# Kernel tuning notes

Hardware: AMD Instinct MI355X
Metric: run time of the kernel (lower is better)

Reference implementation:

```python
import jax, jax.numpy as jnp
import numpy as np

N, E, B = 400000, 800000, 16384
MAX_DEG = 10  # PyG MFConv default max_degree -> 11 weight sets
EPS = 1e-5


def setup_inputs() -> dict:
    key = jax.random.key(0)
    ks = jax.random.split(key, 32)
    d = {}
    d["x"] = jax.random.normal(ks[0], (N, 8), jnp.float32)
    d["edge_index"] = jax.random.randint(ks[1], (2, E), 0, N)
    d["batch"] = jnp.sort(jax.random.randint(ks[2], (N,), 0, B))
    d["x_mord"] = jax.random.normal(ks[3], (B, 862), jnp.float32)
    D = MAX_DEG + 1
    # MFConv degree-dependent weights: Wl (with bias) applied to neighbor sum, Wr (no bias) to self.
    d["Wl1"] = jax.random.normal(ks[4], (D, 32, 8), jnp.float32) * 0.2
    d["bl1"] = jnp.zeros((D, 32), jnp.float32)
    d["Wr1"] = jax.random.normal(ks[5], (D, 32, 8), jnp.float32) * 0.2
    d["Wl2"] = jax.random.normal(ks[6], (D, 32, 32), jnp.float32) * 0.1
    d["bl2"] = jnp.zeros((D, 32), jnp.float32)
    d["Wr2"] = jax.random.normal(ks[7], (D, 32, 32), jnp.float32) * 0.1
    d["Wl3"] = jax.random.normal(ks[8], (D, 32, 32), jnp.float32) * 0.1
    d["bl3"] = jnp.zeros((D, 32), jnp.float32)
    d["Wr3"] = jax.random.normal(ks[9], (D, 32, 32), jnp.float32) * 0.1
    # Dense MLP head
    d["W_fc1"] = jax.random.normal(ks[10], (512, 862), jnp.float32) * 0.03
    d["b_fc1"] = jnp.zeros((512,), jnp.float32)
    d["g1"] = jnp.ones((512,), jnp.float32)
    d["be1"] = jnp.zeros((512,), jnp.float32)
    d["W_fc2"] = jax.random.normal(ks[11], (128, 512), jnp.float32) * 0.04
    d["b_fc2"] = jnp.zeros((128,), jnp.float32)
    d["g2"] = jnp.ones((128,), jnp.float32)
    d["be2"] = jnp.zeros((128,), jnp.float32)
    d["W_fc3"] = jax.random.normal(ks[12], (64, 128), jnp.float32) * 0.09
    d["b_fc3"] = jnp.zeros((64,), jnp.float32)
    d["g3"] = jnp.ones((64,), jnp.float32)
    d["be3"] = jnp.zeros((64,), jnp.float32)
    d["W_out"] = jax.random.normal(ks[13], (1, 96), jnp.float32) * 0.1
    d["b_out"] = jnp.zeros((1,), jnp.float32)
    return d


def _mfconv(x, src, dst, deg_idx, Wl, bl, Wr):
    # h_i = sum_{j in N(i)} x_j  (source_to_target aggregation)
    h = jax.ops.segment_sum(x[src], dst, num_segments=x.shape[0])
    Wl_n = Wl[deg_idx]   # [N, out, in]
    Wr_n = Wr[deg_idx]
    return (jnp.einsum('noi,ni->no', Wl_n, h) + bl[deg_idx]
            + jnp.einsum('noi,ni->no', Wr_n, x))


def _bn_train(h, g, b):
    mu = jnp.mean(h, axis=0)
    var = jnp.mean((h - mu) ** 2, axis=0)  # biased, as torch BN training
    return (h - mu) * jax.lax.rsqrt(var + EPS) * g + b


def reference(x, edge_index, batch, x_mord,
              Wl1, bl1, Wr1, Wl2, bl2, Wr2, Wl3, bl3, Wr3,
              W_fc1, b_fc1, g1, be1, W_fc2, b_fc2, g2, be2,
              W_fc3, b_fc3, g3, be3, W_out, b_out):
    src, dst = edge_index[0], edge_index[1]
    n = x.shape[0]
    deg = jax.ops.segment_sum(jnp.ones((src.shape[0],), jnp.float32), dst, num_segments=n)
    deg_idx = jnp.minimum(deg, MAX_DEG).astype(jnp.int32)

    h = jax.nn.relu(_mfconv(x, src, dst, deg_idx, Wl1, bl1, Wr1))
    h = jax.nn.relu(_mfconv(h, src, dst, deg_idx, Wl2, bl2, Wr2))
    h = _mfconv(h, src, dst, deg_idx, Wl3, bl3, Wr3)

    # global mean pool over graphs
    num_graphs = x_mord.shape[0]
    sums = jax.ops.segment_sum(h, batch, num_segments=num_graphs)
    cnts = jax.ops.segment_sum(jnp.ones((n,), jnp.float32), batch, num_segments=num_graphs)
    pooled = sums / jnp.maximum(cnts, 1.0)[:, None]  # [B, 32]

    m = _bn_train(jax.nn.relu(x_mord @ W_fc1.T + b_fc1), g1, be1)
    m = _bn_train(jax.nn.relu(m @ W_fc2.T + b_fc2), g2, be2)
    m = _bn_train(jax.nn.relu(m @ W_fc3.T + b_fc3), g3, be3)

    z = jnp.concatenate([pooled, m], axis=1)  # [B, 96]
    return jax.nn.sigmoid(z @ W_out.T + b_out)
```

## Files before the change

kernel.cpp:

```cpp
#include <hip/hip_runtime.h>
#include <hip/hip_bf16.h>
#include <math.h>

#define MORD 862

typedef short s16x8 __attribute__((ext_vector_type(8)));
typedef float f32x4 __attribute__((ext_vector_type(4)));
typedef float f32x4a __attribute__((ext_vector_type(4), aligned(4)));

static __device__ __forceinline__ unsigned short f2bf(float v) {
  __hip_bfloat16 h = __float2bfloat16(v);
  return *(unsigned short*)&h;
}
static __device__ __forceinline__ float bf2f(unsigned short u) {
  unsigned int x = ((unsigned int)u) << 16;
  return *(float*)&x;
}

__global__ __launch_bounds__(512) void bin_scan(const int* __restrict__ bhist, int* __restrict__ boff,
                                                int* __restrict__ gcur, int nbins, int E) {
  __shared__ int ts[512];
  int tid = threadIdx.x;
  int v = (tid < nbins) ? bhist[tid] : 0;
  ts[tid] = v;
  __syncthreads();
  for (int st = 1; st < 512; st <<= 1) {
    int t = (tid >= st) ? ts[tid - st] : 0;
    __syncthreads();
    ts[tid] += t;
    __syncthreads();
  }
  int ex = ts[tid] - v;
  if (tid < nbins) { boff[tid] = ex; gcur[tid] = ex; }
  if (tid == 0) boff[nbins] = E;
}

__global__ __launch_bounds__(256) void bin_split(const int* __restrict__ srcA, const int* __restrict__ dstA,
                                                 int* __restrict__ gcur, unsigned long long* __restrict__ ebuf,
                                                 int E, int nbins) {
  __shared__ unsigned long long sbuf[512 * 8];
  __shared__ int lcur[512];
  int tid = threadIdx.x;
  for (int base = blockIdx.x * 1024; base < E; base += (int)gridDim.x * 1024) {
    for (int i = tid; i < nbins; i += 256) lcur[i] = 0;
    __syncthreads();
    int e0 = base + tid * 4;
#pragma unroll
    for (int j = 0; j < 4; j++) {
      int e = e0 + j;
      if (e < E) {
        int d = dstA[e], s = srcA[e];
        int bin = d >> 10;
        unsigned long long p = ((unsigned long long)(unsigned int)d << 32) | (unsigned int)s;
        int slot = atomicAdd(&lcur[bin], 1);
        if (slot < 8) sbuf[bin * 8 + slot] = p;
        else { int g = atomicAdd(&gcur[bin], 1); ebuf[g] = p; }
      }
    }
    __syncthreads();
    for (int b = tid; b < nbins; b += 256) {
      int cnt = min(lcur[b], 8);
      if (cnt > 0) {
        int g = atomicAdd(&gcur[b], cnt);
        for (int k = 0; k < cnt; k++) ebuf[g + k] = sbuf[b * 8 + k];
      }
    }
    __syncthreads();
  }
}

__global__ __launch_bounds__(256) void bin_csr(const unsigned long long* __restrict__ ebuf,
                                               const int* __restrict__ boff,
                                               int* __restrict__ off, int* __restrict__ csr,
                                               int N, int E) {
  __shared__ int lcur[1024];
  __shared__ int part[256];
  int b = blockIdx.x;
  int n0 = b << 10;
  int nn = min(1024, N - n0);
  int e0 = boff[b], e1 = boff[b + 1];
  int tid = threadIdx.x;
  for (int i = tid; i < nn; i += 256) lcur[i] = 0;
  __syncthreads();
  for (int e = e0 + tid; e < e1; e += 256) {
    int d = (int)(ebuf[e] >> 32);
    atomicAdd(&lcur[d - n0], 1);
  }
  __syncthreads();
  int base4 = tid * 4;
  int c0 = (base4 < nn) ? lcur[base4] : 0;
  int c1 = (base4 + 1 < nn) ? lcur[base4 + 1] : 0;
  int c2 = (base4 + 2 < nn) ? lcur[base4 + 2] : 0;
  int c3 = (base4 + 3 < nn) ? lcur[base4 + 3] : 0;
  int tot = c0 + c1 + c2 + c3;
  part[tid] = tot;
  __syncthreads();
  for (int st = 1; st < 256; st <<= 1) {
    int t = (tid >= st) ? part[tid - st] : 0;
    __syncthreads();
    part[tid] += t;
    __syncthreads();
  }
  int pre = part[tid] - tot;
  __syncthreads();
  if (base4 < nn)     { lcur[base4]     = pre;                off[n0 + base4]     = e0 + pre; }
  if (base4 + 1 < nn) { lcur[base4 + 1] = pre + c0;           off[n0 + base4 + 1] = e0 + pre + c0; }
  if (base4 + 2 < nn) { lcur[base4 + 2] = pre + c0 + c1;      off[n0 + base4 + 2] = e0 + pre + c0 + c1; }
  if (base4 + 3 < nn) { lcur[base4 + 3] = pre + c0 + c1 + c2; off[n0 + base4 + 3] = e0 + pre + c0 + c1 + c2; }
  if (b == 0 && tid == 0) off[N] = E;
  __syncthreads();
  for (int e = e0 + tid; e < e1; e += 256) {
    unsigned long long p = ebuf[e];
    int d = (int)(p >> 32);
    int s = (int)(p & 0xffffffffu);
    int slot = atomicAdd(&lcur[d - n0], 1);
    csr[e0 + slot] = s;
  }
}

__global__ __launch_bounds__(256) void mega_prep(const int* __restrict__ dstA, int* __restrict__ bhist, int E, int nbins,
                                                 const float* __restrict__ Wl1, const float* __restrict__ Wr1,
                                                 unsigned short* __restrict__ Wc1,
                                                 const float* __restrict__ Wl2, const float* __restrict__ Wr2,
                                                 unsigned short* __restrict__ Wc2,
                                                 const float* __restrict__ Wl3, const float* __restrict__ Wr3,
                                                 unsigned short* __restrict__ Wc3,
                                                 const int* __restrict__ batch, int* __restrict__ goff, int N, int B,
                                                 const float* __restrict__ Wf1, unsigned short* __restrict__ Bbf1) {
  if (blockIdx.y == 0) {
    if (blockIdx.x >= 400) return;
    __shared__ int lh[512];
    for (int i = threadIdx.x; i < nbins; i += 256) lh[i] = 0;
    __syncthreads();
    for (int e = blockIdx.x * 256 + threadIdx.x; e < E; e += 400 * 256)
      atomicAdd(&lh[dstA[e] >> 10], 1);
    __syncthreads();
    for (int i = threadIdx.x; i < nbins; i += 256)
      if (lh[i]) atomicAdd(&bhist[i], lh[i]);
    return;
  }
  int bx = blockIdx.x;
  if (bx >= 330) {
    int idx = (bx - 330) * 256 + threadIdx.x;
    if (idx >= 512 * 224) return;
    int r = idx / 224, c4 = (idx % 224) * 4;
#pragma unroll
    for (int j = 0; j < 4; j++) {
      int k = c4 + j;
      float v = (k < MORD) ? Wf1[(size_t)r * MORD + k] : 0.f;
      Bbf1[(size_t)r * 896 + k] = f2bf(v);
    }
    return;
  }
  if (bx >= 264) {
    int b = (bx - 264) * 256 + threadIdx.x;
    if (b > B) return;
    int lo = 0, hi = N;
    while (lo < hi) {
      int mid = (lo + hi) >> 1;
      if (batch[mid] < b) lo = mid + 1; else hi = mid;
    }
    goff[b] = lo;
    return;
  }
  int set = bx / 88;
  const float* Wl = set == 0 ? Wl1 : (set == 1 ? Wl2 : Wl3);
  const float* Wr = set == 0 ? Wr1 : (set == 1 ? Wr2 : Wr3);
  unsigned short* Wc = set == 0 ? Wc1 : (set == 1 ? Wc2 : Wc3);
  int CIN = set == 0 ? 8 : 32;
  int idx = (bx - set * 88) * 256 + threadIdx.x;
  if (idx >= 352 * 64) return;
  int row = idx >> 6, k = idx & 63;
  int d = row >> 5, o = row & 31;
  float v = 0.f;
  if (k < CIN) v = Wl[((size_t)d * 32 + o) * CIN + k];
  else if (k < 2 * CIN) v = Wr[((size_t)d * 32 + o) * CIN + (k - CIN)];
  Wc[idx] = f2bf(v);
}

__global__ __launch_bounds__(256) void prep_hx1(const float* __restrict__ x, const int* __restrict__ off,
                                                const int* __restrict__ csr,
                                                unsigned short* __restrict__ x1, unsigned short* __restrict__ agg1, int N) {
  int n = blockIdx.x * 256 + threadIdx.x;
  if (n >= N) return;
  int a = off[n], b = off[n + 1];
  float ag[8] = {};
  for (int base = a; base < b; base += 4) {
    int rem = b - base;
    int j1 = base + (rem > 1 ? 1 : 0);
    int j2 = base + (rem > 2 ? 2 : 0);
    int j3 = base + (rem > 3 ? 3 : 0);
    int cc0 = csr[base], cc1 = csr[j1], cc2 = csr[j2], cc3 = csr[j3];
    f32x4a v0a = *(const f32x4a*)(x + (size_t)cc0 * 8);
    f32x4a v0b = *(const f32x4a*)(x + (size_t)cc0 * 8 + 4);
    f32x4a v1a = *(const f32x4a*)(x + (size_t)cc1 * 8);
    f32x4a v1b = *(const f32x4a*)(x + (size_t)cc1 * 8 + 4);
    f32x4a v2a = *(const f32x4a*)(x + (size_t)cc2 * 8);
    f32x4a v2b = *(const f32x4a*)(x + (size_t)cc2 * 8 + 4);
    f32x4a v3a = *(const f32x4a*)(x + (size_t)cc3 * 8);
    f32x4a v3b = *(const f32x4a*)(x + (size_t)cc3 * 8 + 4);
    float m1 = rem > 1 ? 1.f : 0.f;
    float m2 = rem > 2 ? 1.f : 0.f;
    float m3 = rem > 3 ? 1.f : 0.f;
#pragma unroll
    for (int t = 0; t < 4; t++) {
      ag[t] += v0a[t];
      ag[t] = fmaf(m1, v1a[t], ag[t]);
      ag[t] = fmaf(m2, v2a[t], ag[t]);
      ag[t] = fmaf(m3, v3a[t], ag[t]);
      ag[t + 4] += v0b[t];
      ag[t + 4] = fmaf(m1, v1b[t], ag[t + 4]);
      ag[t + 4] = fmaf(m2, v2b[t], ag[t + 4]);
      ag[t + 4] = fmaf(m3, v3b[t], ag[t + 4]);
    }
  }
  const float* xo = x + (size_t)n * 8;
  s16x8 w0, w1;
#pragma unroll
  for (int t = 0; t < 8; t++) {
    w0[t] = (short)f2bf(ag[t]);
    w1[t] = (short)f2bf(xo[t]);
  }
  *(s16x8*)(agg1 + (size_t)n * 8) = w0;
  *(s16x8*)(x1 + (size_t)n * 8) = w1;
}

__global__ __launch_bounds__(256) void gather_c(const unsigned short* __restrict__ X, const int* __restrict__ off,
                                                const int* __restrict__ csr, unsigned short* __restrict__ AGG, int N) {
  long long tid = (long long)blockIdx.x * 256 + threadIdx.x;
  if (tid >= (long long)N * 4) return;
  int n = (int)(tid >> 2), q = (int)(tid & 3);
  int a = off[n], b = off[n + 1];
  float s[8] = {};
  for (int base = a; base < b; base += 4) {
    int rem = b - base;
    int j1 = base + (rem > 1 ? 1 : 0);
    int j2 = base + (rem > 2 ? 2 : 0);
    int j3 = base + (rem > 3 ? 3 : 0);
    int cc0 = csr[base], cc1 = csr[j1], cc2 = csr[j2], cc3 = csr[j3];
    const s16x8 v0 = *(const s16x8*)(X + (size_t)cc0 * 32 + q * 8);
    const s16x8 v1 = *(const s16x8*)(X + (size_t)cc1 * 32 + q * 8);
    const s16x8 v2 = *(const s16x8*)(X + (size_t)cc2 * 32 + q * 8);
    const s16x8 v3 = *(const s16x8*)(X + (size_t)cc3 * 32 + q * 8);
    float m1 = rem > 1 ? 1.f : 0.f;
    float m2 = rem > 2 ? 1.f : 0.f;
    float m3 = rem > 3 ? 1.f : 0.f;
#pragma unroll
    for (int t = 0; t < 8; t++) {
      s[t] += bf2f((unsigned short)v0[t]);
      s[t] = fmaf(m1, bf2f((unsigned short)v1[t]), s[t]);
      s[t] = fmaf(m2, bf2f((unsigned short)v2[t]), s[t]);
      s[t] = fmaf(m3, bf2f((unsigned short)v3[t]), s[t]);
    }
  }
  s16x8 w;
#pragma unroll
  for (int t = 0; t < 8; t++) w[t] = (short)f2bf(s[t]);
  *(s16x8*)(AGG + (size_t)n * 32 + q * 8) = w;
}

template <int KS, int ACH, int OUTMODE>
__global__ __launch_bounds__(512, 4) void mfconv_mfma(const unsigned short* __restrict__ xin,
                                                      const unsigned short* __restrict__ agg,
                                                      const unsigned short* __restrict__ Wcat,
                                                      const float* __restrict__ bl,
                                                      const int* __restrict__ off,
                                                      unsigned short* __restrict__ outp, int N) {
  __shared__ __align__(16) unsigned short As[128 * ACH * 8];
  __shared__ __align__(16) unsigned short Bs[352 * 64];
  __shared__ float sbias[352];
  __shared__ int sdeg[128];
  const int tid = threadIdx.x;
  const int wid = tid >> 6, lane = tid & 63;

  for (int s = wid; s < 44; s += 8) {
    int c = s * 64 + lane;
    int cs = c ^ ((c >> 3) & 7);
    __builtin_amdgcn_global_load_lds((const __attribute__((address_space(1))) void*)((const char*)Wcat + (size_t)cs * 16),
                                     (__attribute__((address_space(3))) void*)((char*)Bs + s * 1024), 16, 0, 0);
  }
  for (int i = tid; i < 352; i += 512) sbias[i] = bl[i];

  const int ntiles = N >> 7;
  for (int t = blockIdx.x; t < ntiles; t += (int)gridDim.x) {
    const int row0 = t << 7;
    __syncthreads();
    for (int s = wid; s < 2 * ACH; s += 8) {
      int c = s * 64 + lane;
      int row = c / ACH, ch = c & (ACH - 1);
      int cs = ch ^ (row & (ACH - 1));
      size_t grow = (size_t)(row0 + row);
      const char* srcp;
      if (ACH == 4) {
        srcp = (cs == 1) ? (const char*)xin + grow * 16 : (const char*)agg + grow * 16;
      } else {
        srcp = (cs < 4) ? (const char*)agg + grow * 64 + (size_t)cs * 16
                        : (const char*)xin + grow * 64 + (size_t)(cs - 4) * 16;
      }
      __builtin_amdgcn_global_load_lds((const __attribute__((address_space(1))) void*)srcp,
                                       (__attribute__((address_space(3))) void*)((char*)As + s * 1024), 16, 0, 0);
    }
    if (tid < 128) sdeg[tid] = min(off[row0 + tid + 1] - off[row0 + tid], 10);
    __syncthreads();

    const int ra = wid * 16 + (lane & 15);
    const int g4 = lane >> 4;
    const int rl0 = wid * 16 + g4 * 4;
    int dj[4];
#pragma unroll
    for (int j = 0; j < 4; j++) dj[j] = sdeg[rl0 + j];

#pragma unroll
    for (int h = 0; h < 2; h++) {
      f32x4 acc[11] = {};
#pragma unroll
      for (int kk = 0; kk < KS; kk++) {
        int cha = (kk * 4 + g4) ^ (ra & (ACH - 1));
        s16x8 af = *(const s16x8*)((const char*)As + (size_t)(ra * ACH + cha) * 16);
#pragma unroll
        for (int nn = 0; nn < 11; nn++) {
          int rb = (h * 11 + nn) * 16 + (lane & 15);
          int cb = rb * 8 + kk * 4 + g4;
          s16x8 bf = *(const s16x8*)((const char*)Bs + (size_t)(cb ^ (rb & 7)) * 16);
          acc[nn] = __builtin_amdgcn_mfma_f32_16x16x32_bf16(af, bf, acc[nn], 0, 0, 0);
        }
      }
#pragma unroll
      for (int nn = 0; nn < 11; nn++) {
        int n = h * 11 + nn;
        int dsel = n >> 1;
        int o = (n & 1) * 16 + (lane & 15);
        float bv = sbias[dsel * 32 + o];
#pragma unroll
        for (int j = 0; j < 4; j++) {
          if (dj[j] == dsel) {
            float v = acc[nn][j] + bv;
            size_t gr = (size_t)row0 + rl0 + j;
            if (OUTMODE == 0) v = fmaxf(v, 0.f);
            outp[gr * 32 + o] = f2bf(v);
          }
        }
      }
    }
  }
}

__global__ __launch_bounds__(256) void cvtA(const float* __restrict__ xm, unsigned short* __restrict__ Abf, int B) {
  const int q = 224;
  int t = blockIdx.x * 256 + threadIdx.x;
  if (t >= B * q) return;
  int r = t / q, c4 = (t % q) * 4;
#pragma unroll
  for (int j = 0; j < 4; j++) {
    int k = c4 + j;
    float v = (k < MORD) ? xm[(size_t)r * MORD + k] : 0.f;
    Abf[(size_t)r * 896 + k] = f2bf(v);
  }
}

__global__ __launch_bounds__(256) void gemm_fc1b(const unsigned short* __restrict__ A,
                                                 const unsigned short* __restrict__ Bw,
                                                 const float* __restrict__ bias,
                                                 unsigned short* __restrict__ Cout,
                                                 float* __restrict__ csum, float* __restrict__ csq,
                                                 int M, int Nn, int Kp) {
  __shared__ __align__(16) unsigned short As[128 * 64];
  __shared__ __align__(16) unsigned short Bs[128 * 64];
  __shared__ float scs[128], sqs[128];
  int tid = threadIdx.x;
  int wid = tid >> 6, lane = tid & 63;
  int lin = blockIdx.x + blockIdx.y * 4;
  int swz = (lin & 7) * 64 + (lin >> 3);
  int m0 = (swz >> 2) * 128, n0 = (swz & 3) * 128;
  int wr = wid >> 1, wc = wid & 1;
  f32x4 acc[4][4] = {};

  int srow_l = lane >> 3;
  int scol = (lane & 7) * 8;
  int aReadBase = ((wr * 64 + (lane & 15)) * 128) + ((lane >> 4) * 16);
  int bReadBase = ((wc * 64 + (lane & 15)) * 128) + ((lane >> 4) * 16);

  const unsigned short* Ablk = A + (size_t)m0 * Kp;
  const unsigned short* Bblk = Bw + (size_t)n0 * Kp;

  for (int k0 = 0; k0 < Kp; k0 += 64) {
#pragma unroll
    for (int i = 0; i < 4; i++) {
      int s = wid * 4 + i;
      int row = s * 8 + srow_l;
      const unsigned short* ga = Ablk + (size_t)row * Kp + k0 + scol;
      const unsigned short* gb = Bblk + (size_t)row * Kp + k0 + scol;
      __builtin_amdgcn_global_load_lds((const __attribute__((address_space(1))) void*)ga,
                                       (__attribute__((address_space(3))) void*)(As + s * 512), 16, 0, 0);
      __builtin_amdgcn_global_load_lds((const __attribute__((address_space(1))) void*)gb,
                                       (__attribute__((address_space(3))) void*)(Bs + s * 512), 16, 0, 0);
    }
    __syncthreads();
#pragma unroll
    for (int kk = 0; kk < 2; kk++) {
      s16x8 af[4], bfr[4];
#pragma unroll
      for (int m = 0; m < 4; m++)
        af[m] = *(const s16x8*)((const char*)As + aReadBase + m * (16 * 128) + kk * 64);
#pragma unroll
      for (int n = 0; n < 4; n++)
        bfr[n] = *(const s16x8*)((const char*)Bs + bReadBase + n * (16 * 128) + kk * 64);
#pragma unroll
      for (int m = 0; m < 4; m++)
#pragma unroll
        for (int n = 0; n < 4; n++)
          acc[m][n] = __builtin_amdgcn_mfma_f32_16x16x32_bf16(af[m], bfr[n], acc[m][n], 0, 0, 0);
    }
    __syncthreads();
  }

  if (tid < 128) { scs[tid] = 0.f; sqs[tid] = 0.f; }
  __syncthreads();
  int rbase = m0 + wr * 64 + (lane >> 4) * 4;
  int lc = lane & 15;
#pragma unroll
  for (int n = 0; n < 4; n++) {
    int colb = wc * 64 + n * 16 + lc;
    float bv = bias[n0 + colb];
    float s = 0.f, q = 0.f;
#pragma unroll
    for (int m = 0; m < 4; m++) {
#pragma unroll
      for (int j = 0; j < 4; j++) {
        int row = rbase + m * 16 + j;
        float v = fmaxf(acc[m][n][j] + bv, 0.f);
        Cout[(size_t)row * Nn + n0 + colb] = f2bf(v);
        s += v;
        q = fmaf(v, v, q);
      }
    }
    s += __shfl_xor(s, 16); q += __shfl_xor(q, 16);
    s += __shfl_xor(s, 32); q += __shfl_xor(q, 32);
    if ((lane >> 4) == 0) { atomicAdd(&scs[colb], s); atomicAdd(&sqs[colb], q); }
  }
  __syncthreads();
  if (tid < 128) { atomicAdd(&csum[n0 + tid], scs[tid]); atomicAdd(&csq[n0 + tid], sqs[tid]); }
}

__global__ __launch_bounds__(256) void prepW2_bn(const float* __restrict__ W2, const float* __restrict__ b2,
                                                 const float* __restrict__ s1, const float* __restrict__ q1,
                                                 const float* __restrict__ g1, const float* __restrict__ be1,
                                                 unsigned short* __restrict__ W2p, float* __restrict__ b2p,
                                                 int Nn, int K, float invM) {
  __shared__ float a1l[512], h1l[512];
  for (int c = threadIdx.x; c < K; c += 256) {
    float mu = s1[c] * invM;
    float var = q1[c] * invM - mu * mu;
    float sc = g1[c] * rsqrtf(var + 1e-5f);
    a1l[c] = sc;
    h1l[c] = be1[c] - mu * sc;
  }
  __syncthreads();
  int wid = threadIdx.x >> 6, lane = threadIdx.x & 63;
  int n = blockIdx.x * 4 + wid;
  if (n >= Nn) return;
  float part = 0.f;
  for (int k = lane; k < K; k += 64) {
    float w = W2[(size_t)n * K + k];
    W2p[(size_t)n * K + k] = f2bf(w * a1l[k]);
    part = fmaf(w, h1l[k], part);
  }
#pragma unroll
  for (int off = 32; off > 0; off >>= 1) part += __shfl_down(part, off, 64);
  if (lane == 0) b2p[n] = b2[n] + part;
}

__global__ __launch_bounds__(256) void gemm_fc2(const unsigned short* __restrict__ A,
                                                const unsigned short* __restrict__ Bw,
                                                const float* __restrict__ bias,
                                                float* __restrict__ Cout,
                                                float* __restrict__ csum, float* __restrict__ csq,
                                                int M, int Nn, int Kp) {
  __shared__ __align__(16) unsigned short As[128 * 64];
  __shared__ __align__(16) unsigned short Bs[128 * 64];
  __shared__ float scs[128], sqs[128];
  int tid = threadIdx.x;
  int wid = tid >> 6, lane = tid & 63;
  int m0 = blockIdx.y * 128;
  int wr = wid >> 1, wc = wid & 1;
  f32x4 acc[4][4] = {};

  int srow_l = lane >> 3;
  int scol = (lane & 7) * 8;
  int aReadBase = ((wr * 64 + (lane & 15)) * 128) + ((lane >> 4) * 16);
  int bReadBase = ((wc * 64 + (lane & 15)) * 128) + ((lane >> 4) * 16);

  const unsigned short* Ablk = A + (size_t)m0 * Kp;

  for (int k0 = 0; k0 < Kp; k0 += 64) {
#pragma unroll
    for (int i = 0; i < 4; i++) {
      int s = wid * 4 + i;
      int row = s * 8 + srow_l;
      const unsigned short* ga = Ablk + (size_t)row * Kp + k0 + scol;
      const unsigned short* gb = Bw + (size_t)row * Kp + k0 + scol;
      __builtin_amdgcn_global_load_lds((const __attribute__((address_space(1))) void*)ga,
                                       (__attribute__((address_space(3))) void*)(As + s * 512), 16, 0, 0);
      __builtin_amdgcn_global_load_lds((const __attribute__((address_space(1))) void*)gb,
                                       (__attribute__((address_space(3))) void*)(Bs + s * 512), 16, 0, 0);
    }
    __syncthreads();
#pragma unroll
    for (int kk = 0; kk < 2; kk++) {
      s16x8 af[4], bfr[4];
#pragma unroll
      for (int m = 0; m < 4; m++)
        af[m] = *(const s16x8*)((const char*)As + aReadBase + m * (16 * 128) + kk * 64);
#pragma unroll
      for (int n = 0; n < 4; n++)
        bfr[n] = *(const s16x8*)((const char*)Bs + bReadBase + n * (16 * 128) + kk * 64);
#pragma unroll
      for (int m = 0; m < 4; m++)
#pragma unroll
        for (int n = 0; n < 4; n++)
          acc[m][n] = __builtin_amdgcn_mfma_f32_16x16x32_bf16(af[m], bfr[n], acc[m][n], 0, 0, 0);
    }
    __syncthreads();
  }

  if (tid < 128) { scs[tid] = 0.f; sqs[tid] = 0.f; }
  __syncthreads();
  int rbase = m0 + wr * 64 + (lane >> 4) * 4;
  int lc = lane & 15;
#pragma unroll
  for (int n = 0; n < 4; n++) {
    int colb = wc * 64 + n * 16 + lc;
    float bv = bias[colb];
    float s = 0.f, q = 0.f;
#pragma unroll
    for (int m = 0; m < 4; m++) {
#pragma unroll
      for (int j = 0; j < 4; j++) {
        int row = rbase + m * 16 + j;
        float v = fmaxf(acc[m][n][j] + bv, 0.f);
        Cout[(size_t)row * Nn + colb] = v;
        s += v;
        q = fmaf(v, v, q);
      }
    }
    s += __shfl_xor(s, 16); q += __shfl_xor(q, 16);
    s += __shfl_xor(s, 32); q += __shfl_xor(q, 32);
    if ((lane >> 4) == 0) { atomicAdd(&scs[colb], s); atomicAdd(&sqs[colb], q); }
  }
  __syncthreads();
  if (tid < 128) { atomicAdd(&csum[tid], scs[tid]); atomicAdd(&csq[tid], sqs[tid]); }
}

__global__ __launch_bounds__(256) void gemm_fc3(const float* __restrict__ A, const float* __restrict__ Bw,
                                                const float* __restrict__ bias,
                                                const float* __restrict__ s2v, const float* __restrict__ q2v,
                                                const float* __restrict__ g2, const float* __restrict__ be2,
                                                float* __restrict__ C, float* __restrict__ s3, float* __restrict__ q3,
                                                int M, float invM) {
  const int BM = 64, BN = 64, BK = 16, K = 128;
  __shared__ float As[BK][BM + 1];
  __shared__ float Bs[BK][BN + 1];
  __shared__ float a2l[128], h2l[128];
  __shared__ float scs[64], sqs[64];
  int tid = threadIdx.x;
  for (int c = tid; c < 128; c += 256) {
    float mu = s2v[c] * invM;
    float var = q2v[c] * invM - mu * mu;
    float sc = g2[c] * rsqrtf(var + 1e-5f);
    a2l[c] = sc;
    h2l[c] = be2[c] - mu * sc;
  }
  if (tid < 64) { scs[tid] = 0.f; sqs[tid] = 0.f; }
  __syncthreads();
  int bm = blockIdx.y * BM;
  int tr = tid / 16, tc = tid % 16;
  float acc[4][4] = {};
  for (int k0 = 0; k0 < K; k0 += BK) {
    for (int i = tid; i < BM * BK; i += 256) {
      int m = i / BK, k = i % BK;
      float v = A[(size_t)(bm + m) * K + k0 + k];
      As[k][m] = fmaf(v, a2l[k0 + k], h2l[k0 + k]);
    }
    for (int i = tid; i < BN * BK; i += 256) {
      int n = i / BK, k = i % BK;
      Bs[k][n] = Bw[(size_t)n * K + k0 + k];
    }
    __syncthreads();
#pragma unroll
    for (int k = 0; k < BK; k++) {
      float a4[4], b4[4];
#pragma unroll
      for (int xx = 0; xx < 4; xx++) a4[xx] = As[k][tr * 4 + xx];
#pragma unroll
      for (int yy = 0; yy < 4; yy++) b4[yy] = Bs[k][tc * 4 + yy];
#pragma unroll
      for (int xx = 0; xx < 4; xx++)
#pragma unroll
        for (int yy = 0; yy < 4; yy++) acc[xx][yy] = fmaf(a4[xx], b4[yy], acc[xx][yy]);
    }
    __syncthreads();
  }
#pragma unroll
  for (int yy = 0; yy < 4; yy++) {
    int n = tc * 4 + yy;
    float bv = bias[n];
    float s = 0.f, q = 0.f;
#pragma unroll
    for (int xx = 0; xx < 4; xx++) {
      int m = bm + tr * 4 + xx;
      float v = fmaxf(acc[xx][yy] + bv, 0.f);
      C[(size_t)m * 64 + n] = v;
      s += v;
      q = fmaf(v, v, q);
    }
    atomicAdd(&scs[n], s);
    atomicAdd(&sqs[n], q);
  }
  __syncthreads();
  if (tid < 64) { atomicAdd(&s3[tid], scs[tid]); atomicAdd(&q3[tid], sqs[tid]); }
}

__global__ __launch_bounds__(256) void pool_head(const unsigned short* __restrict__ H3, const int* __restrict__ goff,
                                                 const float* __restrict__ m3,
                                                 const float* __restrict__ s3, const float* __restrict__ q3,
                                                 const float* __restrict__ g3, const float* __restrict__ be3,
                                                 const float* __restrict__ Wout, const float* __restrict__ bout,
                                                 float* __restrict__ out, int B, float invM) {
  __shared__ float a3l[64], h3l[64];
  if (threadIdx.x < 64) {
    int c = threadIdx.x;
    float mu = s3[c] * invM;
    float var = q3[c] * invM - mu * mu;
    float sc = g3[c] * rsqrtf(var + 1e-5f);
    a3l[c] = sc;
    h3l[c] = be3[c] - mu * sc;
  }
  __syncthreads();
  int w = (int)((blockIdx.x * 256 + threadIdx.x) >> 6);
  if (w >= B) return;
  int lane = threadIdx.x & 63;
  int c = lane & 31, r2 = lane >> 5;
  int a = goff[w], b = goff[w + 1];
  float s = 0.f;
  for (int r = a + r2; r < b; r += 2) s += bf2f(H3[(size_t)r * 32 + c]);
  s += __shfl_down(s, 32);
  float val = 0.f;
  if (r2 == 0) val = (s / fmaxf((float)(b - a), 1.f)) * Wout[c];
  float mv = m3[(size_t)w * 64 + lane];
  val += fmaf(mv, a3l[lane], h3l[lane]) * Wout[32 + lane];
#pragma unroll
  for (int off = 32; off > 0; off >>= 1) val += __shfl_down(val, off);
  if (lane == 0) out[w] = 1.f / (1.f + expf(-(val + bout[0])));
}

extern "C" void kernel_launch(void* const* d_in, const int* in_sizes, int n_in,
                              void* d_out, int out_size, void* d_ws, size_t ws_size,
                              hipStream_t stream) {
  const float* x = (const float*)d_in[0];
  const int* eidx = (const int*)d_in[1];
  const int* batch = (const int*)d_in[2];
  const float* xmord = (const float*)d_in[3];
  const float* Wl1 = (const float*)d_in[4];
  const float* bl1 = (const float*)d_in[5];
  const float* Wr1 = (const float*)d_in[6];
  const float* Wl2 = (const float*)d_in[7];
  const float* bl2 = (const float*)d_in[8];
  const float* Wr2 = (const float*)d_in[9];
  const float* Wl3 = (const float*)d_in[10];
  const float* bl3 = (const float*)d_in[11];
  const float* Wr3 = (const float*)d_in[12];
  const float* Wf1 = (const float*)d_in[13];
  const float* bf1 = (const float*)d_in[14];
  const float* g1 = (const float*)d_in[15];
  const float* be1 = (const float*)d_in[16];
  const float* Wf2 = (const float*)d_in[17];
  const float* bf2 = (const float*)d_in[18];
  const float* g2 = (const float*)d_in[19];
  const float* be2 = (const float*)d_in[20];
  const float* Wf3 = (const float*)d_in[21];
  const float* bf3 = (const float*)d_in[22];
  const float* g3 = (const float*)d_in[23];
  const float* be3 = (const float*)d_in[24];
  const float* Wout = (const float*)d_in[25];
  const float* bout = (const float*)d_in[26];
  float* out = (float*)d_out;

  const int N = in_sizes[2];
  const int E = in_sizes[1] / 2;
  const int B = in_sizes[3] / MORD;
  const int nbins = (N + 1023) >> 10;
  const int* src = eidx;
  const int* dst = eidx + E;

  char* ws = (char*)d_ws;
  size_t off_ = 0;
  auto alloc = [&](size_t bytes) { size_t o = off_; off_ += (bytes + 255) & ~(size_t)255; return o; };
  size_t oX1 = alloc((size_t)N * 8 * 2);
  size_t oAGG1 = alloc((size_t)N * 8 * 2);
  size_t oX2 = alloc((size_t)N * 32 * 2);
  size_t oX3 = alloc((size_t)N * 32 * 2);
  size_t oAGG = alloc((size_t)N * 32 * 2);
  size_t oOff = alloc((size_t)(N + 1) * 4);
  size_t oCsr = alloc((size_t)E * 4);
  size_t oEbuf = alloc((size_t)E * 8);
  size_t oH3 = alloc((size_t)N * 32 * 2);
  size_t oGoff = alloc((size_t)(B + 1) * 4);
  size_t oStats = alloc(8192 * 4);
  size_t oWc1 = alloc(352 * 64 * 2);
  size_t oWc2 = alloc(352 * 64 * 2);
  size_t oWc3 = alloc(352 * 64 * 2);
  size_t oBbf1 = alloc(512 * 896 * 2);
  size_t oW2p = alloc(128 * 512 * 2 + 1024);
  (void)ws_size;

  unsigned short* X1 = (unsigned short*)(ws + oX1);
  unsigned short* AGG1 = (unsigned short*)(ws + oAGG1);
  unsigned short* X2 = (unsigned short*)(ws + oX2);
  unsigned short* X3 = (unsigned short*)(ws + oX3);
  unsigned short* AGG = (unsigned short*)(ws + oAGG);
  int* offp = (int*)(ws + oOff);
  int* csr = (int*)(ws + oCsr);
  unsigned long long* ebuf = (unsigned long long*)(ws + oEbuf);
  unsigned short* H3 = (unsigned short*)(ws + oH3);
  int* goff = (int*)(ws + oGoff);
  float* st = (float*)(ws + oStats);
  int* bhist = (int*)(st + 4096);
  int* boff = (int*)(st + 4608);
  int* gcur = (int*)(st + 5184);
  unsigned short* Wc1 = (unsigned short*)(ws + oWc1);
  unsigned short* Wc2 = (unsigned short*)(ws + oWc2);
  unsigned short* Wc3 = (unsigned short*)(ws + oWc3);
  unsigned short* Bbf1 = (unsigned short*)(ws + oBbf1);
  unsigned short* W2p = (unsigned short*)(ws + oW2p);
  float* b2p = (float*)(ws + oW2p + 131072);
  float *s1 = st, *q1 = st + 512;
  float *s2 = st + 2048, *q2 = st + 2176;
  float *s3 = st + 2560, *q3 = st + 2624;

  unsigned short* Abf = (unsigned short*)(ws + oX2);
  unsigned short* m1 = (unsigned short*)(ws + oAGG);
  float* m2 = (float*)(ws + oAGG + 16777216);
  float* m3 = (float*)(ws + oOff);

  hipMemsetAsync(st, 0, 4608 * 4, stream);

  mega_prep<<<dim3(778, 2), 256, 0, stream>>>(dst, bhist, E, nbins,
                                              Wl1, Wr1, Wc1, Wl2, Wr2, Wc2, Wl3, Wr3, Wc3,
                                              batch, goff, N, B, Wf1, Bbf1);
  bin_scan<<<1, 512, 0, stream>>>(bhist, boff, gcur, nbins, E);
  bin_split<<<400, 256, 0, stream>>>(src, dst, gcur, ebuf, E, nbins);
  bin_csr<<<nbins, 256, 0, stream>>>(ebuf, boff, offp, csr, N, E);

  prep_hx1<<<(N + 255) / 256, 256, 0, stream>>>(x, offp, csr, X1, AGG1, N);
  mfconv_mfma<1, 4, 0><<<512, 512, 0, stream>>>(X1, AGG1, Wc1, bl1, offp, X2, N);
  gather_c<<<(int)(((long long)N * 4 + 255) / 256), 256, 0, stream>>>(X2, offp, csr, AGG, N);
  mfconv_mfma<2, 8, 0><<<512, 512, 0, stream>>>(X2, AGG, Wc2, bl2, offp, X3, N);
  gather_c<<<(int)(((long long)N * 4 + 255) / 256), 256, 0, stream>>>(X3, offp, csr, AGG, N);
  mfconv_mfma<2, 8, 1><<<512, 512, 0, stream>>>(X3, AGG, Wc3, bl3, offp, H3, N);

  cvtA<<<(B * 224 + 255) / 256, 256, 0, stream>>>(xmord, Abf, B);
  gemm_fc1b<<<dim3(4, B / 128), 256, 0, stream>>>(Abf, Bbf1, bf1, m1, s1, q1, B, 512, 896);
  prepW2_bn<<<32, 256, 0, stream>>>(Wf2, bf2, s1, q1, g1, be1, W2p, b2p, 128, 512, 1.f / B);
  gemm_fc2<<<dim3(1, B / 128), 256, 0, stream>>>(m1, W2p, b2p, m2, s2, q2, B, 128, 512);
  gemm_fc3<<<dim3(1, B / 64), 256, 0, stream>>>(m2, Wf3, bf3, s2, q2, g2, be2, m3, s3, q3, B, 1.f / B);
  pool_head<<<(B * 64 + 255) / 256, 256, 0, stream>>>(H3, goff, m3, s3, q3, g3, be3, Wout, bout, out, B, 1.f / B);
}
```

Before: 327.0 us.

## Sort nodes by degree so MFConv tiles compute only needed weight sets

Adds a degree histogram in bin_csr, a tiny scan, and a permutation kernel that groups nodes by clamped degree. The MFConv MFMA kernels then load rows through this permutation and loop only over the degree range present in each 128-row tile, instead of computing all 11 weight sets and masking. This cuts MFMA work about elevenfold, at the cost of two extra launches, indirect gathers for A rows, and scattered output stores.

```diff
diff --git a/kernel.cpp b/kernel.cpp
--- a/kernel.cpp
+++ b/kernel.cpp
@@ -72,15 +72,18 @@
 __global__ __launch_bounds__(256) void bin_csr(const unsigned long long* __restrict__ ebuf,
                                                const int* __restrict__ boff,
                                                int* __restrict__ off, int* __restrict__ csr,
+                                               int* __restrict__ dcnt,
                                                int N, int E) {
   __shared__ int lcur[1024];
   __shared__ int part[256];
+  __shared__ int ldc[11];
   int b = blockIdx.x;
   int n0 = b << 10;
   int nn = min(1024, N - n0);
   int e0 = boff[b], e1 = boff[b + 1];
   int tid = threadIdx.x;
   for (int i = tid; i < nn; i += 256) lcur[i] = 0;
+  if (tid < 11) ldc[tid] = 0;
   __syncthreads();
   for (int e = e0 + tid; e < e1; e += 256) {
     int d = (int)(ebuf[e] >> 32);
@@ -93,6 +96,10 @@
   int c2 = (base4 + 2 < nn) ? lcur[base4 + 2] : 0;
   int c3 = (base4 + 3 < nn) ? lcur[base4 + 3] : 0;
   int tot = c0 + c1 + c2 + c3;
+  if (base4 < nn) atomicAdd(&ldc[min(c0, 10)], 1);
+  if (base4 + 1 < nn) atomicAdd(&ldc[min(c1, 10)], 1);
+  if (base4 + 2 < nn) atomicAdd(&ldc[min(c2, 10)], 1);
+  if (base4 + 3 < nn) atomicAdd(&ldc[min(c3, 10)], 1);
   part[tid] = tot;
   __syncthreads();
   for (int st = 1; st < 256; st <<= 1) {
@@ -109,12 +116,52 @@
   if (base4 + 3 < nn) { lcur[base4 + 3] = pre + c0 + c1 + c2; off[n0 + base4 + 3] = e0 + pre + c0 + c1 + c2; }
   if (b == 0 && tid == 0) off[N] = E;
   __syncthreads();
+  if (tid < 11 && ldc[tid]) atomicAdd(&dcnt[tid], ldc[tid]);
   for (int e = e0 + tid; e < e1; e += 256) {
     unsigned long long p = ebuf[e];
     int d = (int)(p >> 32);
     int s = (int)(p & 0xffffffffu);
     int slot = atomicAdd(&lcur[d - n0], 1);
     csr[e0 + slot] = s;
+  }
+}
+
+__global__ void scan11(const int* __restrict__ dcnt, int* __restrict__ dcur) {
+  if (threadIdx.x == 0) {
+    int run = 0;
+    for (int d = 0; d < 11; d++) { dcur[d] = run; run += dcnt[d]; }
+  }
+}
+
+__global__ __launch_bounds__(256) void perm_scatter(const int* __restrict__ off, int* __restrict__ dcur,
+                                                    int* __restrict__ perm, int* __restrict__ degp, int N) {
+  __shared__ int ldc[11];
+  __shared__ int lbase[11];
+  int tid = threadIdx.x;
+  if (tid < 11) ldc[tid] = 0;
+  __syncthreads();
+  int n0 = blockIdx.x * 1024;
+  int d[4], slot[4];
+#pragma unroll
+  for (int j = 0; j < 4; j++) {
+    int n = n0 + tid * 4 + j;
+    d[j] = -1;
+    if (n < N) {
+      d[j] = min(off[n + 1] - off[n], 10);
+      slot[j] = atomicAdd(&ldc[d[j]], 1);
+    }
+  }
+  __syncthreads();
+  if (tid < 11) lbase[tid] = ldc[tid] ? atomicAdd(&dcur[tid], ldc[tid]) : 0;
+  __syncthreads();
+#pragma unroll
+  for (int j = 0; j < 4; j++) {
+    int n = n0 + tid * 4 + j;
+    if (n < N) {
+      int p = lbase[d[j]] + slot[j];
+      perm[p] = n;
+      degp[p] = d[j];
+    }
   }
 }
 
@@ -264,12 +311,12 @@
                                                       const unsigned short* __restrict__ agg,
                                                       const unsigned short* __restrict__ Wcat,
                                                       const float* __restrict__ bl,
-                                                      const int* __restrict__ off,
+                                                      const int* __restrict__ perm,
+                                                      const int* __restrict__ degp,
                                                       unsigned short* __restrict__ outp, int N) {
   __shared__ __align__(16) unsigned short As[128 * ACH * 8];
   __shared__ __align__(16) unsigned short Bs[352 * 64];
   __shared__ float sbias[352];
-  __shared__ int sdeg[128];
   const int tid = threadIdx.x;
   const int wid = tid >> 6, lane = tid & 63;
 
@@ -281,6 +328,11 @@
   }
   for (int i = tid; i < 352; i += 512) sbias[i] = bl[i];
 
+  const int ra = wid * 16 + (lane & 15);
+  const int g4 = lane >> 4;
+  const int lc = lane & 15;
+  const int rl0 = wid * 16 + g4 * 4;
+
   const int ntiles = N >> 7;
   for (int t = blockIdx.x; t < ntiles; t += (int)gridDim.x) {
     const int row0 = t << 7;
@@ -289,56 +341,52 @@
       int c = s * 64 + lane;
       int row = c / ACH, ch = c & (ACH - 1);
       int cs = ch ^ (row & (ACH - 1));
-      size_t grow = (size_t)(row0 + row);
+      size_t g = (size_t)perm[row0 + row];
       const char* srcp;
       if (ACH == 4) {
-        srcp = (cs == 1) ? (const char*)xin + grow * 16 : (const char*)agg + grow * 16;
+        srcp = (cs == 1) ? (const char*)xin + g * 16 : (const char*)agg + g * 16;
       } else {
-        srcp = (cs < 4) ? (const char*)agg + grow * 64 + (size_t)cs * 16
-                        : (const char*)xin + grow * 64 + (size_t)(cs - 4) * 16;
+        srcp = (cs < 4) ? (const char*)agg + g * 64 + (size_t)cs * 16
+                        : (const char*)xin + g * 64 + (size_t)(cs - 4) * 16;
       }
       __builtin_amdgcn_global_load_lds((const __attribute__((address_space(1))) void*)srcp,
                                        (__attribute__((address_space(3))) void*)((char*)As + s * 1024), 16, 0, 0);
     }
-    if (tid < 128) sdeg[tid] = min(off[row0 + tid + 1] - off[row0 + tid], 10);
-    __syncthreads();
-
-    const int ra = wid * 16 + (lane & 15);
-    const int g4 = lane >> 4;
-    const int rl0 = wid * 16 + g4 * 4;
-    int dj[4];
-#pragma unroll
-    for (int j = 0; j < 4; j++) dj[j] = sdeg[rl0 + j];
-
-#pragma unroll
-    for (int h = 0; h < 2; h++) {
-      f32x4 acc[11] = {};
+    int dj[4], pj[4];
+#pragma unroll
+    for (int j = 0; j < 4; j++) {
+      int rr = row0 + rl0 + j;
+      dj[j] = degp[rr];
+      pj[j] = perm[rr];
+    }
+    int dmin = degp[row0], dmax = degp[row0 + 127];
+    __syncthreads();
+
+    s16x8 af[KS];
+#pragma unroll
+    for (int kk = 0; kk < KS; kk++) {
+      int cha = (kk * 4 + g4) ^ (ra & (ACH - 1));
+      af[kk] = *(const s16x8*)((const char*)As + (size_t)(ra * ACH + cha) * 16);
+    }
+
+    for (int nn2 = dmin * 2; nn2 <= dmax * 2 + 1; nn2++) {
+      f32x4 acc = {};
+      int rb = nn2 * 16 + lc;
 #pragma unroll
       for (int kk = 0; kk < KS; kk++) {
-        int cha = (kk * 4 + g4) ^ (ra & (ACH - 1));
-        s16x8 af = *(const s16x8*)((const char*)As + (size_t)(ra * ACH + cha) * 16);
-#pragma unroll
-        for (int nn = 0; nn < 11; nn++) {
-          int rb = (h * 11 + nn) * 16 + (lane & 15);
-          int cb = rb * 8 + kk * 4 + g4;
-          s16x8 bf = *(const s16x8*)((const char*)Bs + (size_t)(cb ^ (rb & 7)) * 16);
-          acc[nn] = __builtin_amdgcn_mfma_f32_16x16x32_bf16(af, bf, acc[nn], 0, 0, 0);
-        }
+        int cb = rb * 8 + kk * 4 + g4;
+        s16x8 bf = *(const s16x8*)((const char*)Bs + (size_t)(cb ^ (rb & 7)) * 16);
+        acc = __builtin_amdgcn_mfma_f32_16x16x32_bf16(af[kk], bf, acc, 0, 0, 0);
       }
-#pragma unroll
-      for (int nn = 0; nn < 11; nn++) {
-        int n = h * 11 + nn;
-        int dsel = n >> 1;
-        int o = (n & 1) * 16 + (lane & 15);
-        float bv = sbias[dsel * 32 + o];
-#pragma unroll
-        for (int j = 0; j < 4; j++) {
-          if (dj[j] == dsel) {
-            float v = acc[nn][j] + bv;
-            size_t gr = (size_t)row0 + rl0 + j;
-            if (OUTMODE == 0) v = fmaxf(v, 0.f);
-            outp[gr * 32 + o] = f2bf(v);
-          }
+      int dsel = nn2 >> 1;
+      int o = (nn2 & 1) * 16 + lc;
+      float bv = sbias[dsel * 32 + o];
+#pragma unroll
+      for (int j = 0; j < 4; j++) {
+        if (dj[j] == dsel) {
+          float v = acc[j] + bv;
+          if (OUTMODE == 0) v = fmaxf(v, 0.f);
+          outp[(size_t)pj[j] * 32 + o] = f2bf(v);
         }
       }
     }
@@ -711,6 +759,8 @@
   size_t oWc3 = alloc(352 * 64 * 2);
   size_t oBbf1 = alloc(512 * 896 * 2);
   size_t oW2p = alloc(128 * 512 * 2 + 1024);
+  size_t oPerm = alloc((size_t)N * 4);
+  size_t oDegp = alloc((size_t)N * 4);
   (void)ws_size;
 
   unsigned short* X1 = (unsigned short*)(ws + oX1);
@@ -727,12 +777,16 @@
   int* bhist = (int*)(st + 4096);
   int* boff = (int*)(st + 4608);
   int* gcur = (int*)(st + 5184);
+  int* dcnt = (int*)(st + 5696);
+  int* dcur = (int*)(st + 5728);
   unsigned short* Wc1 = (unsigned short*)(ws + oWc1);
   unsigned short* Wc2 = (unsigned short*)(ws + oWc2);
   unsigned short* Wc3 = (unsigned short*)(ws + oWc3);
   unsigned short* Bbf1 = (unsigned short*)(ws + oBbf1);
   unsigned short* W2p = (unsigned short*)(ws + oW2p);
   float* b2p = (float*)(ws + oW2p + 131072);
+  int* perm = (int*)(ws + oPerm);
+  int* degp = (int*)(ws + oDegp);
   float *s1 = st, *q1 = st + 512;
   float *s2 = st + 2048, *q2 = st + 2176;
   float *s3 = st + 2560, *q3 = st + 2624;
@@ -742,21 +796,23 @@
   float* m2 = (float*)(ws + oAGG + 16777216);
   float* m3 = (float*)(ws + oOff);
 
-  hipMemsetAsync(st, 0, 4608 * 4, stream);
+  hipMemsetAsync(st, 0, 5728 * 4, stream);
 
   mega_prep<<<dim3(778, 2), 256, 0, stream>>>(dst, bhist, E, nbins,
                                               Wl1, Wr1, Wc1, Wl2, Wr2, Wc2, Wl3, Wr3, Wc3,
                                               batch, goff, N, B, Wf1, Bbf1);
   bin_scan<<<1, 512, 0, stream>>>(bhist, boff, gcur, nbins, E);
   bin_split<<<400, 256, 0, stream>>>(src, dst, gcur, ebuf, E, nbins);
-  bin_csr<<<nbins, 256, 0, stream>>>(ebuf, boff, offp, csr, N, E);
+  bin_csr<<<nbins, 256, 0, stream>>>(ebuf, boff, offp, csr, dcnt, N, E);
+  scan11<<<1, 64, 0, stream>>>(dcnt, dcur);
+  perm_scatter<<<(N + 1023) / 1024, 256, 0, stream>>>(offp, dcur, perm, degp, N);
 
   prep_hx1<<<(N + 255) / 256, 256, 0, stream>>>(x, offp, csr, X1, AGG1, N);
-  mfconv_mfma<1, 4, 0><<<512, 512, 0, stream>>>(X1, AGG1, Wc1, bl1, offp, X2, N);
+  mfconv_mfma<1, 4, 0><<<512, 512, 0, stream>>>(X1, AGG1, Wc1, bl1, perm, degp, X2, N);
   gather_c<<<(int)(((long long)N * 4 + 255) / 256), 256, 0, stream>>>(X2, offp, csr, AGG, N);
-  mfconv_mfma<2, 8, 0><<<512, 512, 0, stream>>>(X2, AGG, Wc2, bl2, offp, X3, N);
+  mfconv_mfma<2, 8, 0><<<512, 512, 0, stream>>>(X2, AGG, Wc2, bl2, perm, degp, X3, N);
   gather_c<<<(int)(((long long)N * 4 + 255) / 256), 256, 0, stream>>>(X3, offp, csr, AGG, N);
-  mfconv_mfma<2, 8, 1><<<512, 512, 0, stream>>>(X3, AGG, Wc3, bl3, offp, H3, N);
+  mfconv_mfma<2, 8, 1><<<512, 512, 0, stream>>>(X3, AGG, Wc3, bl3, perm, degp, H3, N);
 
   cvtA<<<(B * 224 + 255) / 256, 256, 0, stream>>>(xmord, Abf, B);
   gemm_fc1b<<<dim3(4, B / 128), 256, 0, stream>>>(Abf, Bbf1, bf1, m1, s1, q1, B, 512, 896);
```

New measurement: 315.1 us. -3.6%, faster.
